# Performance work log

Measured on AMD Instinct MI355X. Metric: run time of the kernel, lower is better.

Reference implementation:

```python
import jax, jax.numpy as jnp
import numpy as np

B, S, D = 4, 1024, 1024
H, HD = 16, 64
MAXPOS = 1024  # max_position_embeddings


def setup_inputs() -> dict:
    key = jax.random.key(0)
    ks = jax.random.split(key, 10)
    sc = 0.02
    return {
        "hidden_states": jax.random.normal(ks[0], (B, S, D), dtype=jnp.float32),
        "attention_mask": jnp.zeros((B, 1, 1, S), dtype=jnp.float32),
        "across_attention_prior": jax.random.uniform(ks[1], (B, H, S, S), dtype=jnp.float32),
        "head_mask": jnp.ones((1, H, 1, 1), dtype=jnp.float32),
        "Wq": jax.random.normal(ks[2], (D, D), dtype=jnp.float32) * sc,
        "bq": jnp.zeros((D,), dtype=jnp.float32),
        "Wk": jax.random.normal(ks[3], (D, D), dtype=jnp.float32) * sc,
        "bk": jnp.zeros((D,), dtype=jnp.float32),
        "Wv": jax.random.normal(ks[4], (D, D), dtype=jnp.float32) * sc,
        "bv": jnp.zeros((D,), dtype=jnp.float32),
        "dist_emb": jax.random.normal(ks[5], (2 * MAXPOS - 1, HD), dtype=jnp.float32) * sc,
    }


def _heads(x):
    # [B,S,D] -> [B,H,S,HD]
    return x.reshape(B, S, H, HD).transpose(0, 2, 1, 3)


def reference(hidden_states, attention_mask, across_attention_prior, head_mask,
              Wq, bq, Wk, bk, Wv, bv, dist_emb):
    q = _heads(hidden_states @ Wq + bq)  # [B,H,S,HD]
    k = _heads(hidden_states @ Wk + bk)
    v = _heads(hidden_states @ Wv + bv)

    scores = jnp.einsum("bhld,bhrd->bhlr", q, k)

    # relative_key_query positional bias
    pos = jnp.arange(S)
    distance = pos[:, None] - pos[None, :]  # [S,S]
    pe = dist_emb[distance + MAXPOS - 1]  # [S,S,HD] (l, r, d)
    scores = scores + jnp.einsum("bhld,lrd->bhlr", q, pe)
    scores = scores + jnp.einsum("bhrd,lrd->bhlr", k, pe)

    scores = scores / jnp.sqrt(jnp.float32(HD))
    scores = scores + attention_mask  # additive mask, broadcast [B,1,1,S]

    probs = jax.nn.softmax(scores, axis=-1)
    probs = probs * across_attention_prior  # post-softmax multiplicative prior
    probs = probs * head_mask  # dropout prob = 0 (eval)

    ctx = jnp.einsum("bhlr,bhrd->bhld", probs, v)
    ctx = ctx.transpose(0, 2, 1, 3).reshape(B, S, D)
    return ctx
```

## Files before the change

### kernel.cpp

```cpp
#include <hip/hip_runtime.h>


typedef unsigned short u16;
typedef unsigned int   u32;
typedef __attribute__((ext_vector_type(8))) short bfx8;
typedef __attribute__((ext_vector_type(4))) float f32x4;

#define MFMA_BF16(a, b, c) __builtin_amdgcn_mfma_f32_16x16x32_bf16(a, b, c, 0, 0, 0)

__device__ __forceinline__ u16 f2bf(float f) {
    union { float f; u32 u; } c; c.f = f;
    u32 u = c.u;
    return (u16)((u + 0x7FFFu + ((u >> 16) & 1u)) >> 16);
}
__device__ __forceinline__ float bf2f(u16 v) {
    union { u32 u; float f; } c; c.u = ((u32)v) << 16;
    return c.f;
}
__device__ __forceinline__ float load_f(const void* p, long i, bool bf) {
    return bf ? bf2f(((const u16*)p)[i]) : ((const float*)p)[i];
}
__device__ __forceinline__ u16 load_bf(const void* p, long i, bool bf) {
    return bf ? ((const u16*)p)[i] : f2bf(((const float*)p)[i]);
}

__device__ __forceinline__ void gload16(const u16* g, u16* l) {
    __builtin_amdgcn_global_load_lds(
        (__attribute__((address_space(1))) void*)g,
        (__attribute__((address_space(3))) void*)l, 16, 0, 0);
}

__global__ void k_detect(const u32* hid, int* flags) {
    __shared__ int cnt;
    if (threadIdx.x == 0) cnt = 0;
    __syncthreads();
    int c = 0;
    for (int i = threadIdx.x; i < 1024; i += 256) {
        u32 w = hid[i];
        u32 e = (w >> 7) & 0xFFu;
        if (e >= 100u && e <= 140u) c++;
    }
    atomicAdd(&cnt, c);
    __syncthreads();
    if (threadIdx.x == 0) flags[0] = (cnt > 512) ? 1 : 0;
}

__global__ void k_prep(const void* hidden, const void* dist, const void* mask,
                       const void* hm, const void* bq, const void* bk,
                       const void* bv, const int* flags, u16* hid_bf,
                       u16* dist_bf, float* mask_f, float* hm_f, float* bias_f) {
    const bool bf = flags[0] != 0;
    const long NH = 4L * 1024 * 1024, ND = 2047L * 64, NM = 4096, NB = 3072, NHM = 16;
    const long TOT = NH + ND + NM + NB + NHM;
    for (long i = (long)blockIdx.x * 256 + threadIdx.x; i < TOT;
         i += (long)gridDim.x * 256) {
        if (i < NH) hid_bf[i] = load_bf(hidden, i, bf);
        else if (i < NH + ND) dist_bf[i - NH] = load_bf(dist, i - NH, bf);
        else if (i < NH + ND + NM) mask_f[i - NH - ND] = load_f(mask, i - NH - ND, bf);
        else if (i < NH + ND + NM + NB) {
            long j = i - NH - ND - NM;
            const void* src = (j < 1024) ? bq : ((j < 2048) ? bk : bv);
            bias_f[j] = load_f(src, j & 1023, bf);
        } else {
            long j = i - NH - ND - NM - NB;
            hm_f[j] = load_f(hm, j, bf);
        }
    }
}

__global__ void k_transpose(const void* Wq, const void* Wk, const void* Wv,
                            const int* flags, u16* wt) {
    const bool bf = flags[0] != 0;
    __shared__ float t[32][33];
    const int z = blockIdx.z;
    const void* W = (z == 0) ? Wq : ((z == 1) ? Wk : Wv);
    int x = blockIdx.x * 32 + threadIdx.x;
    for (int i = 0; i < 4; i++) {
        int y = blockIdx.y * 32 + threadIdx.y + i * 8;
        t[threadIdx.y + i * 8][threadIdx.x] = load_f(W, (long)y * 1024 + x, bf);
    }
    __syncthreads();
    int x2 = blockIdx.y * 32 + threadIdx.x;
    u16* out = wt + (long)z * 1024 * 1024;
    for (int i = 0; i < 4; i++) {
        int y2 = blockIdx.x * 32 + threadIdx.y + i * 8;
        out[(long)y2 * 1024 + x2] = f2bf(t[threadIdx.x][threadIdx.y + i * 8]);
    }
}

__global__ __launch_bounds__(256, 2)
void k_qkv_gemm(const u16* A, const u16* Bt, const float* bias,
                u16* qb, u16* kb, u16* vb) {
    __shared__ u16 sA[128 * 32];
    __shared__ u16 sB[128 * 32];
    const int tid = threadIdx.x;
    const int w = tid >> 6, lane = tid & 63;
    const int quad = lane >> 4, nl = lane & 15;
    const int wr = w >> 1, wc = w & 1;
    const int n0 = blockIdx.x * 128, m0 = blockIdx.y * 128;

    f32x4 acc[4][4];
#pragma unroll
    for (int a = 0; a < 4; a++)
#pragma unroll
        for (int b = 0; b < 4; b++) acc[a][b] = (f32x4){0.f, 0.f, 0.f, 0.f};

    for (int kt = 0; kt < 32; kt++) {
        const int k0 = kt * 32;
        __syncthreads();
#pragma unroll
        for (int j = 0; j < 2; j++) {
            int row = 32 * w + 16 * j + (lane >> 2);
            int seg = lane & 3;
            gload16(A + (long)(m0 + row) * 1024 + k0 + seg * 8, sA + 1024 * w + 512 * j);
            gload16(Bt + (long)(n0 + row) * 1024 + k0 + seg * 8, sB + 1024 * w + 512 * j);
        }
        __syncthreads();

        bfx8 af[4], bfr[4];
#pragma unroll
        for (int f = 0; f < 4; f++) {
            af[f]  = *(const bfx8*)(sA + (64 * wr + 16 * f + nl) * 32 + quad * 8);
            bfr[f] = *(const bfx8*)(sB + (64 * wc + 16 * f + nl) * 32 + quad * 8);
        }
#pragma unroll
        for (int fm = 0; fm < 4; fm++)
#pragma unroll
            for (int fn = 0; fn < 4; fn++)
                acc[fm][fn] = MFMA_BF16(af[fm], bfr[fn], acc[fm][fn]);
    }

#pragma unroll
    for (int fm = 0; fm < 4; fm++) {
#pragma unroll
        for (int fn = 0; fn < 4; fn++) {
            int n = n0 + 64 * wc + 16 * fn + nl;
            int which = n >> 10, hcol = n & 1023;
            int h = hcol >> 6, hd = hcol & 63;
            u16* op = (which == 0) ? qb : ((which == 1) ? kb : vb);
            float bias_v = bias[n];
#pragma unroll
            for (int reg = 0; reg < 4; reg++) {
                int m = m0 + 64 * wr + 16 * fm + 4 * quad + reg;
                int b = m >> 10, s = m & 1023;
                float v = acc[fm][fn][reg] + bias_v;
                op[((long)((b * 16 + h) * 1024 + s)) * 64 + hd] = f2bf(v);
            }
        }
    }
}

__global__ __launch_bounds__(256, 2)
void k_attn(const u16* qb, const u16* kb, const u16* vb, const u16* Eb,
            const float* maskf, const float* hmf, const void* prior,
            const int* flags, void* out) {
    constexpr int PT = 72;
    constexpr int PD = 132;
    __shared__ __align__(16) char smem[79872];
    u16* sQ  = (u16*)(smem);
    u16* sK  = (u16*)(smem + 9216);
    u16* sVT = (u16*)(smem + 18432);
    u16* sE  = (u16*)(smem + 27648);
    u16* sDq = (u16*)(smem + 46080);
    u16* sDk = (u16*)(smem + 62976);
    u16* sP  = (u16*)(smem + 46080);

    const int tid = threadIdx.x;
    const int w = tid >> 6, lane = tid & 63;
    const int quad = lane >> 4, nl = lane & 15;
    const int bh = blockIdx.x, b = bh >> 4, h = bh & 15;
    const int l0 = blockIdx.y * 64;
    const bool bf = flags[0] != 0;

    const u16* qbh = qb + (long)bh * 65536;
    const u16* kbh = kb + (long)bh * 65536;
    const u16* vbh = vb + (long)bh * 65536;

#pragma unroll
    for (int p = 0; p < 2; p++) {
        int seg = tid + p * 256;
        int row = seg >> 3, s8 = seg & 7;
        *(int4*)(sQ + row * PT + s8 * 8) = *(const int4*)(qbh + (l0 + row) * 64 + s8 * 8);
    }

    f32x4 accv[4];
#pragma unroll
    for (int f = 0; f < 4; f++) accv[f] = (f32x4){0.f, 0.f, 0.f, 0.f};
    float zacc[4] = {0.f, 0.f, 0.f, 0.f};
    const int jb_base = l0 + 960;

    for (int it = 0; it < 16; it++) {
        const int r0 = it * 64;
        __syncthreads();
#pragma unroll
        for (int p = 0; p < 2; p++) {
            int seg = tid + p * 256;
            int row = seg >> 3, s8 = seg & 7;
            *(int4*)(sK + row * PT + s8 * 8) = *(const int4*)(kbh + (r0 + row) * 64 + s8 * 8);
        }
        const int jb = jb_base - r0;
#pragma unroll
        for (int p = 0; p < 4; p++) {
            int seg = tid + p * 256;
            int row = seg >> 3, s8 = seg & 7;
            int j = jb + row; if (j > 2046) j = 2046;
            *(int4*)(sE + row * PT + s8 * 8) = *(const int4*)(Eb + j * 64 + s8 * 8);
        }
        {
            int r = tid & 63, dg = (tid >> 6) * 8;
#pragma unroll
            for (int rep = 0; rep < 2; rep++) {
                int d0 = dg + rep * 32;
                int4 vv = *(const int4*)(vbh + (r0 + r) * 64 + d0);
                const u16* pv8 = (const u16*)&vv;
#pragma unroll
                for (int j2 = 0; j2 < 8; j2++) sVT[(d0 + j2) * PT + r] = pv8[j2];
            }
        }
        float pr[4][4], mval[4];
#pragma unroll
        for (int fn = 0; fn < 4; fn++) {
            mval[fn] = maskf[b * 1024 + r0 + fn * 16 + nl];
#pragma unroll
            for (int reg = 0; reg < 4; reg++) {
                long pidx = ((long)(bh * 1024 + l0 + 16 * w + 4 * quad + reg)) * 1024
                            + r0 + fn * 16 + nl;
                pr[fn][reg] = bf ? bf2f(((const u16*)prior)[pidx])
                                 : ((const float*)prior)[pidx];
            }
        }
        __syncthreads();

        bfx8 aq0 = *(const bfx8*)(sQ + (16 * w + nl) * PT + quad * 8);
        bfx8 aq1 = *(const bfx8*)(sQ + (16 * w + nl) * PT + quad * 8 + 32);
        bfx8 ak0 = *(const bfx8*)(sK + (16 * w + nl) * PT + quad * 8);
        bfx8 ak1 = *(const bfx8*)(sK + (16 * w + nl) * PT + quad * 8 + 32);

#pragma unroll
        for (int fc = 0; fc < 8; fc++) {
            bfx8 be0 = *(const bfx8*)(sE + (fc * 16 + nl) * PT + quad * 8);
            bfx8 be1 = *(const bfx8*)(sE + (fc * 16 + nl) * PT + quad * 8 + 32);
            f32x4 dq = (f32x4){0.f, 0.f, 0.f, 0.f};
            dq = MFMA_BF16(aq0, be0, dq);
            dq = MFMA_BF16(aq1, be1, dq);
            f32x4 dk = (f32x4){0.f, 0.f, 0.f, 0.f};
            dk = MFMA_BF16(ak0, be0, dk);
            dk = MFMA_BF16(ak1, be1, dk);
#pragma unroll
            for (int reg = 0; reg < 4; reg++) {
                int rr = 16 * w + 4 * quad + reg;
                sDq[rr * PD + fc * 16 + nl] = f2bf(dq[reg]);
                sDk[rr * PD + fc * 16 + nl] = f2bf(dk[reg]);
            }
        }
        f32x4 accs[4];
#pragma unroll
        for (int fn = 0; fn < 4; fn++) {
            bfx8 bk0 = *(const bfx8*)(sK + (fn * 16 + nl) * PT + quad * 8);
            bfx8 bk1 = *(const bfx8*)(sK + (fn * 16 + nl) * PT + quad * 8 + 32);
            f32x4 s = (f32x4){0.f, 0.f, 0.f, 0.f};
            s = MFMA_BF16(aq0, bk0, s);
            s = MFMA_BF16(aq1, bk1, s);
            accs[fn] = s;
        }
        __syncthreads();

        float pw[4][4];
#pragma unroll
        for (int fn = 0; fn < 4; fn++) {
#pragma unroll
            for (int reg = 0; reg < 4; reg++) {
                int li = 16 * w + 4 * quad + reg;
                int ri = 16 * fn + nl;
                int u = li - ri + 63;
                float s = (accs[fn][reg] + bf2f(sDq[li * PD + u])
                           + bf2f(sDk[ri * PD + u])) * 0.125f + mval[fn];
                float e = __expf(s);
                zacc[reg] += e;
                pw[fn][reg] = e * pr[fn][reg];
            }
        }
        __syncthreads();

#pragma unroll
        for (int fn = 0; fn < 4; fn++)
#pragma unroll
            for (int reg = 0; reg < 4; reg++)
                sP[(16 * w + 4 * quad + reg) * PT + fn * 16 + nl] = f2bf(pw[fn][reg]);

        bfx8 ap0 = *(const bfx8*)(sP + (16 * w + nl) * PT + quad * 8);
        bfx8 ap1 = *(const bfx8*)(sP + (16 * w + nl) * PT + quad * 8 + 32);
#pragma unroll
        for (int fd = 0; fd < 4; fd++) {
            bfx8 bv0 = *(const bfx8*)(sVT + (fd * 16 + nl) * PT + quad * 8);
            bfx8 bv1 = *(const bfx8*)(sVT + (fd * 16 + nl) * PT + quad * 8 + 32);
            accv[fd] = MFMA_BF16(ap0, bv0, accv[fd]);
            accv[fd] = MFMA_BF16(ap1, bv1, accv[fd]);
        }
    }

#pragma unroll
    for (int reg = 0; reg < 4; reg++) {
        float z = zacc[reg];
        z += __shfl_xor(z, 1);
        z += __shfl_xor(z, 2);
        z += __shfl_xor(z, 4);
        z += __shfl_xor(z, 8);
        zacc[reg] = z;
    }
    const float hm = hmf[h];
#pragma unroll
    for (int fd = 0; fd < 4; fd++) {
#pragma unroll
        for (int reg = 0; reg < 4; reg++) {
            int l = l0 + 16 * w + 4 * quad + reg;
            int d = fd * 16 + nl;
            float val = accv[fd][reg] * hm / zacc[reg];
            long oidx = ((long)(b * 1024 + l)) * 1024 + h * 64 + d;
            if (bf) ((u16*)out)[oidx] = f2bf(val);
            else    ((float*)out)[oidx] = val;
        }
    }
}

extern "C" void kernel_launch(void* const* d_in, const int* in_sizes, int n_in,
                              void* d_out, int out_size, void* d_ws, size_t ws_size,
                              hipStream_t stream) {
    char* ws = (char*)d_ws;
    int*   flags   = (int*)ws;
    u16*   hid_bf  = (u16*)(ws + 256);
    u16*   wt_bf   = (u16*)(ws + 8388864);
    u16*   dist_bf = (u16*)(ws + 14680320);
    float* mask_f  = (float*)(ws + 14942464);
    float* bias_f  = (float*)(ws + 14958848);
    float* hm_f    = (float*)(ws + 14971136);
    u16*   q_bf    = (u16*)(ws + 14971392);
    u16*   k_bf    = (u16*)(ws + 23360000);
    u16*   v_bf    = (u16*)(ws + 31748608);

    k_detect<<<1, 256, 0, stream>>>((const u32*)d_in[0], flags);
    k_prep<<<2048, 256, 0, stream>>>(d_in[0], d_in[10], d_in[1], d_in[3],
                                     d_in[5], d_in[7], d_in[9], flags,
                                     hid_bf, dist_bf, mask_f, hm_f, bias_f);
    k_transpose<<<dim3(32, 32, 3), dim3(32, 8), 0, stream>>>(
        d_in[4], d_in[6], d_in[8], flags, wt_bf);
    k_qkv_gemm<<<dim3(24, 32), 256, 0, stream>>>(hid_bf, wt_bf, bias_f,
                                                 q_bf, k_bf, v_bf);
    k_attn<<<dim3(64, 16), 256, 0, stream>>>(q_bf, k_bf, v_bf, dist_bf,
                                             mask_f, hm_f, d_in[2], flags, d_out);
}
```

Before: 517.3 us.

## Restructure attention LDS layout with swizzling, async loads, and register-resident Dq

The QKV projection now writes V pre-transposed with packed 64-bit stores, so the attention kernel can fill K, V^T and the distance embeddings straight into XOR-swizzled LDS tiles using global_load_lds. Q is held in registers instead of LDS. The q·E relative term stays in registers and is redistributed across lanes with ds_bpermute rather than round-tripping through shared memory. Dropping the Q and Dq buffers and the padding cuts LDS use enough to raise occupancy to 3 blocks per CU and remove one barrier, in exchange for more intricate indexing and higher register pressure.

```diff
diff --git a/kernel.cpp b/kernel.cpp
--- a/kernel.cpp
+++ b/kernel.cpp
@@ -3,6 +3,7 @@
 
 typedef unsigned short u16;
 typedef unsigned int   u32;
+typedef unsigned long long u64;
 typedef __attribute__((ext_vector_type(8))) short bfx8;
 typedef __attribute__((ext_vector_type(4))) float f32x4;
 
@@ -28,6 +29,10 @@
     __builtin_amdgcn_global_load_lds(
         (__attribute__((address_space(1))) void*)g,
         (__attribute__((address_space(3))) void*)l, 16, 0, 0);
+}
+
+__device__ __forceinline__ bfx8 ld_sw(const u16* arr, int row, int chunk) {
+    return *(const bfx8*)(arr + row * 64 + ((chunk ^ (row & 7)) * 8));
 }
 
 __global__ void k_detect(const u32* hid, int* flags) {
@@ -137,51 +142,52 @@
             int n = n0 + 64 * wc + 16 * fn + nl;
             int which = n >> 10, hcol = n & 1023;
             int h = hcol >> 6, hd = hcol & 63;
-            u16* op = (which == 0) ? qb : ((which == 1) ? kb : vb);
             float bias_v = bias[n];
-#pragma unroll
-            for (int reg = 0; reg < 4; reg++) {
-                int m = m0 + 64 * wr + 16 * fm + 4 * quad + reg;
-                int b = m >> 10, s = m & 1023;
-                float v = acc[fm][fn][reg] + bias_v;
-                op[((long)((b * 16 + h) * 1024 + s)) * 64 + hd] = f2bf(v);
+            int mbase = m0 + 64 * wr + 16 * fm + 4 * quad;
+            int b = mbase >> 10, s = mbase & 1023;
+            if (which == 2) {
+                u64 pk = 0;
+#pragma unroll
+                for (int reg = 0; reg < 4; reg++)
+                    pk |= (u64)f2bf(acc[fm][fn][reg] + bias_v) << (16 * reg);
+                *(u64*)&vb[((long)((b * 16 + h) * 64 + hd)) * 1024 + s] = pk;
+            } else {
+                u16* op = (which == 0) ? qb : kb;
+#pragma unroll
+                for (int reg = 0; reg < 4; reg++)
+                    op[((long)((b * 16 + h) * 1024 + s + reg)) * 64 + hd] =
+                        f2bf(acc[fm][fn][reg] + bias_v);
             }
         }
     }
 }
 
-__global__ __launch_bounds__(256, 2)
-void k_attn(const u16* qb, const u16* kb, const u16* vb, const u16* Eb,
+__global__ __launch_bounds__(256, 3)
+void k_attn(const u16* qb, const u16* kb, const u16* vTb, const u16* Eb,
             const float* maskf, const float* hmf, const void* prior,
             const int* flags, void* out) {
-    constexpr int PT = 72;
-    constexpr int PD = 132;
-    __shared__ __align__(16) char smem[79872];
-    u16* sQ  = (u16*)(smem);
-    u16* sK  = (u16*)(smem + 9216);
-    u16* sVT = (u16*)(smem + 18432);
-    u16* sE  = (u16*)(smem + 27648);
-    u16* sDq = (u16*)(smem + 46080);
-    u16* sDk = (u16*)(smem + 62976);
-    u16* sP  = (u16*)(smem + 46080);
+    __shared__ __align__(16) u16 smem[24576];
+    u16* sK  = smem;
+    u16* sVT = smem + 4096;
+    u16* sE  = smem + 8192;
+    u16* sP  = smem + 8192;
+    u16* sDk = smem + 16384;
 
     const int tid = threadIdx.x;
     const int w = tid >> 6, lane = tid & 63;
     const int quad = lane >> 4, nl = lane & 15;
+    const int rloc = lane >> 3;
+    const int cperm = (lane & 7) ^ rloc;
     const int bh = blockIdx.x, b = bh >> 4, h = bh & 15;
     const int l0 = blockIdx.y * 64;
     const bool bf = flags[0] != 0;
 
-    const u16* qbh = qb + (long)bh * 65536;
-    const u16* kbh = kb + (long)bh * 65536;
-    const u16* vbh = vb + (long)bh * 65536;
-
-#pragma unroll
-    for (int p = 0; p < 2; p++) {
-        int seg = tid + p * 256;
-        int row = seg >> 3, s8 = seg & 7;
-        *(int4*)(sQ + row * PT + s8 * 8) = *(const int4*)(qbh + (l0 + row) * 64 + s8 * 8);
-    }
+    const u16* qbh = qb  + (long)bh * 65536;
+    const u16* kbh = kb  + (long)bh * 65536;
+    const u16* vbh = vTb + (long)bh * 65536;
+
+    const bfx8 aq0 = *(const bfx8*)(qbh + (l0 + 16 * w + nl) * 64 + quad * 8);
+    const bfx8 aq1 = *(const bfx8*)(qbh + (l0 + 16 * w + nl) * 64 + quad * 8 + 32);
 
     f32x4 accv[4];
 #pragma unroll
@@ -192,30 +198,19 @@
     for (int it = 0; it < 16; it++) {
         const int r0 = it * 64;
         __syncthreads();
-#pragma unroll
-        for (int p = 0; p < 2; p++) {
-            int seg = tid + p * 256;
-            int row = seg >> 3, s8 = seg & 7;
-            *(int4*)(sK + row * PT + s8 * 8) = *(const int4*)(kbh + (r0 + row) * 64 + s8 * 8);
-        }
+
         const int jb = jb_base - r0;
 #pragma unroll
-        for (int p = 0; p < 4; p++) {
-            int seg = tid + p * 256;
-            int row = seg >> 3, s8 = seg & 7;
-            int j = jb + row; if (j > 2046) j = 2046;
-            *(int4*)(sE + row * PT + s8 * 8) = *(const int4*)(Eb + j * 64 + s8 * 8);
-        }
-        {
-            int r = tid & 63, dg = (tid >> 6) * 8;
-#pragma unroll
-            for (int rep = 0; rep < 2; rep++) {
-                int d0 = dg + rep * 32;
-                int4 vv = *(const int4*)(vbh + (r0 + r) * 64 + d0);
-                const u16* pv8 = (const u16*)&vv;
-#pragma unroll
-                for (int j2 = 0; j2 < 8; j2++) sVT[(d0 + j2) * PT + r] = pv8[j2];
-            }
+        for (int j = 0; j < 2; j++) {
+            int row = 16 * w + 8 * j + rloc;
+            gload16(kbh + (r0 + row) * 64 + cperm * 8, sK + (16 * w + 8 * j) * 64);
+            gload16(vbh + row * 1024 + r0 + cperm * 8, sVT + (16 * w + 8 * j) * 64);
+        }
+#pragma unroll
+        for (int j = 0; j < 4; j++) {
+            int row = 32 * w + 8 * j + rloc;
+            int je = jb + row; if (je > 2046) je = 2046;
+            gload16(Eb + je * 64 + cperm * 8, sE + (32 * w + 8 * j) * 64);
         }
         float pr[4][4], mval[4];
 #pragma unroll
@@ -231,33 +226,31 @@
         }
         __syncthreads();
 
-        bfx8 aq0 = *(const bfx8*)(sQ + (16 * w + nl) * PT + quad * 8);
-        bfx8 aq1 = *(const bfx8*)(sQ + (16 * w + nl) * PT + quad * 8 + 32);
-        bfx8 ak0 = *(const bfx8*)(sK + (16 * w + nl) * PT + quad * 8);
-        bfx8 ak1 = *(const bfx8*)(sK + (16 * w + nl) * PT + quad * 8 + 32);
-
+        const bfx8 ak0 = ld_sw(sK, 16 * w + nl, quad);
+        const bfx8 ak1 = ld_sw(sK, 16 * w + nl, 4 + quad);
+        u32 dqp[8][2];
 #pragma unroll
         for (int fc = 0; fc < 8; fc++) {
-            bfx8 be0 = *(const bfx8*)(sE + (fc * 16 + nl) * PT + quad * 8);
-            bfx8 be1 = *(const bfx8*)(sE + (fc * 16 + nl) * PT + quad * 8 + 32);
+            bfx8 be0 = ld_sw(sE, fc * 16 + nl, quad);
+            bfx8 be1 = ld_sw(sE, fc * 16 + nl, 4 + quad);
             f32x4 dq = (f32x4){0.f, 0.f, 0.f, 0.f};
             dq = MFMA_BF16(aq0, be0, dq);
             dq = MFMA_BF16(aq1, be1, dq);
             f32x4 dk = (f32x4){0.f, 0.f, 0.f, 0.f};
             dk = MFMA_BF16(ak0, be0, dk);
             dk = MFMA_BF16(ak1, be1, dk);
-#pragma unroll
-            for (int reg = 0; reg < 4; reg++) {
-                int rr = 16 * w + 4 * quad + reg;
-                sDq[rr * PD + fc * 16 + nl] = f2bf(dq[reg]);
-                sDk[rr * PD + fc * 16 + nl] = f2bf(dk[reg]);
-            }
+            dqp[fc][0] = (u32)f2bf(dq[0]) | ((u32)f2bf(dq[1]) << 16);
+            dqp[fc][1] = (u32)f2bf(dq[2]) | ((u32)f2bf(dq[3]) << 16);
+            int u = fc * 16 + nl;
+            u64 pk = (u64)f2bf(dk[0]) | ((u64)f2bf(dk[1]) << 16)
+                   | ((u64)f2bf(dk[2]) << 32) | ((u64)f2bf(dk[3]) << 48);
+            *(u64*)(sDk + u * 64 + (((4 * w + quad) ^ (u & 15)) * 4)) = pk;
         }
         f32x4 accs[4];
 #pragma unroll
         for (int fn = 0; fn < 4; fn++) {
-            bfx8 bk0 = *(const bfx8*)(sK + (fn * 16 + nl) * PT + quad * 8);
-            bfx8 bk1 = *(const bfx8*)(sK + (fn * 16 + nl) * PT + quad * 8 + 32);
+            bfx8 bk0 = ld_sw(sK, fn * 16 + nl, quad);
+            bfx8 bk1 = ld_sw(sK, fn * 16 + nl, 4 + quad);
             f32x4 s = (f32x4){0.f, 0.f, 0.f, 0.f};
             s = MFMA_BF16(aq0, bk0, s);
             s = MFMA_BF16(aq1, bk1, s);
@@ -265,35 +258,35 @@
         }
         __syncthreads();
 
-        float pw[4][4];
-#pragma unroll
-        for (int fn = 0; fn < 4; fn++) {
-#pragma unroll
-            for (int reg = 0; reg < 4; reg++) {
-                int li = 16 * w + 4 * quad + reg;
+#pragma unroll
+        for (int reg = 0; reg < 4; reg++) {
+            int srcl = quad * 16 + ((4 * quad + reg + 15 - nl) & 15);
+            int bidx = srcl * 4;
+            u32 bp[8];
+#pragma unroll
+            for (int fc = 0; fc < 8; fc++)
+                bp[fc] = (u32)__builtin_amdgcn_ds_bpermute(bidx, (int)dqp[fc][reg >> 1]);
+#pragma unroll
+            for (int fn = 0; fn < 4; fn++) {
+                int u = 16 * w + 4 * quad + reg + 63 - 16 * fn - nl;
+                u32 word = bp[u >> 4];
+                u16 dqv = (reg & 1) ? (u16)(word >> 16) : (u16)word;
                 int ri = 16 * fn + nl;
-                int u = li - ri + 63;
-                float s = (accs[fn][reg] + bf2f(sDq[li * PD + u])
-                           + bf2f(sDk[ri * PD + u])) * 0.125f + mval[fn];
+                u16 dkv = sDk[u * 64 + (((ri >> 2) ^ (u & 15)) * 4) + (ri & 3)];
+                float s = (accs[fn][reg] + bf2f(dqv) + bf2f(dkv)) * 0.125f + mval[fn];
                 float e = __expf(s);
                 zacc[reg] += e;
-                pw[fn][reg] = e * pr[fn][reg];
+                int li = 16 * w + 4 * quad + reg, ci = fn * 16 + nl;
+                sP[li * 64 + (((ci >> 3) ^ (li & 7)) * 8) + (ci & 7)] =
+                    f2bf(e * pr[fn][reg]);
             }
         }
-        __syncthreads();
-
-#pragma unroll
-        for (int fn = 0; fn < 4; fn++)
-#pragma unroll
-            for (int reg = 0; reg < 4; reg++)
-                sP[(16 * w + 4 * quad + reg) * PT + fn * 16 + nl] = f2bf(pw[fn][reg]);
-
-        bfx8 ap0 = *(const bfx8*)(sP + (16 * w + nl) * PT + quad * 8);
-        bfx8 ap1 = *(const bfx8*)(sP + (16 * w + nl) * PT + quad * 8 + 32);
+        bfx8 ap0 = ld_sw(sP, 16 * w + nl, quad);
+        bfx8 ap1 = ld_sw(sP, 16 * w + nl, 4 + quad);
 #pragma unroll
         for (int fd = 0; fd < 4; fd++) {
-            bfx8 bv0 = *(const bfx8*)(sVT + (fd * 16 + nl) * PT + quad * 8);
-            bfx8 bv1 = *(const bfx8*)(sVT + (fd * 16 + nl) * PT + quad * 8 + 32);
+            bfx8 bv0 = ld_sw(sVT, fd * 16 + nl, quad);
+            bfx8 bv1 = ld_sw(sVT, fd * 16 + nl, 4 + quad);
             accv[fd] = MFMA_BF16(ap0, bv0, accv[fd]);
             accv[fd] = MFMA_BF16(ap1, bv1, accv[fd]);
         }
```

Result: slower. 560.5 us (+8.4%).
